# Kernel optimization log

Measured on AMD Instinct MI355X. Metric: run time of the kernel, lower is better.

Reference implementation:

```python
import jax, jax.numpy as jnp
import numpy as np

N = 20000          # num nodes
E = 250000         # num edges
B = 128            # num graphs in batch
Fin = 512
Fqk = 512
Fv = 512
H = 8              # nheads


def setup_inputs() -> dict:
    key = jax.random.key(0)
    k1, k2, k3, k4 = jax.random.split(key, 4)
    x = jax.random.normal(k1, (N, Fin), dtype=jnp.float32)
    batch = jnp.sort(jax.random.randint(k2, (N,), 0, B)).astype(jnp.int32)
    ei = jax.random.randint(k3, (2, E), 0, N).astype(jnp.int32)
    # proj weight of Linear(Fin, 2*Fqk+Fv, bias=False); stored as (Fin, Ftot)
    W = (jax.random.normal(k4, (Fin, 2 * Fqk + Fv), dtype=jnp.float32)
         / np.sqrt(Fin).astype(np.float32))
    return {"x": x, "batch": batch, "ei": ei, "W": W}


def reference(x, batch, ei, W):
    src, dest = ei[0], ei[1]
    n = x.shape[0]
    Fh = Fqk // H            # head dim for q/k
    Fhv = Fv // H            # head dim for v
    scaling = float(Fh) ** (-0.5)

    qkv = x @ W                                    # (N, 2*Fqk+Fv)
    q, k, v = jnp.split(qkv, [Fqk, 2 * Fqk], axis=-1)
    q = (q * scaling).reshape(n, H, Fh)
    k = k.reshape(n, H, Fh)
    v = v.reshape(n, H, Fhv)

    # edge-wise gathers
    qs = q[src]                                    # (E, H, Fh)
    ks = k[dest]                                   # (E, H, Fh)
    vs = v[dest]                                   # (E, H, Fhv)

    # per-edge, per-head attention scores
    aw = jnp.einsum('ehf,ehf->eh', qs, ks)         # (E, H)

    # segment softmax over edges sharing the same src node (stable)
    m = jax.ops.segment_max(aw, src, num_segments=n)       # (N, H)
    e = jnp.exp(aw - m[src])                                # (E, H)
    denom = jax.ops.segment_sum(e, src, num_segments=n)     # (N, H)
    alpha = e / denom[src]                                   # (E, H)

    # scatter-weighted aggregation of values back to src nodes
    out = jax.ops.segment_sum(alpha[:, :, None] * vs, src, num_segments=n)  # (N, H, Fhv)
    return out.reshape(n, Fv)
```

## Files before the change

### kernel.cpp

```cpp
#include <hip/hip_runtime.h>
#include <cstdint>

typedef float f32x4 __attribute__((ext_vector_type(4)));
typedef __bf16 bf16x8 __attribute__((ext_vector_type(8)));

__device__ __forceinline__ unsigned short f2b(float f) {
  unsigned int u = __float_as_uint(f);
  u = (u + 0x7fffu + ((u >> 16) & 1u)) >> 16;
  return (unsigned short)u;
}

__device__ __forceinline__ void unpack8(uint4 u, float* f) {
  f[0] = __uint_as_float((u.x & 0xffffu) << 16);
  f[1] = __uint_as_float(u.x & 0xffff0000u);
  f[2] = __uint_as_float((u.y & 0xffffu) << 16);
  f[3] = __uint_as_float(u.y & 0xffff0000u);
  f[4] = __uint_as_float((u.z & 0xffffu) << 16);
  f[5] = __uint_as_float(u.z & 0xffff0000u);
  f[6] = __uint_as_float((u.w & 0xffffu) << 16);
  f[7] = __uint_as_float(u.w & 0xffff0000u);
}

__device__ __forceinline__ void async_copy16(const void* g, void* l) {
  __builtin_amdgcn_global_load_lds(
      (const __attribute__((address_space(1))) void*)g,
      (__attribute__((address_space(3))) void*)l, 16, 0, 0);
}

__global__ __launch_bounds__(256) void prep_kernel(
    const float* __restrict__ W, unsigned short* __restrict__ Wt, int NT,
    const int* __restrict__ src, const int* __restrict__ dst,
    int* __restrict__ deg, int* __restrict__ edst, int E, int nbConvw) {
  __shared__ float tile[32][33];
  int bx = blockIdx.x, t = threadIdx.x;

  if (bx < nbConvw) {
    int b = bx;
    int tilesPerRow = NT / 32;
    int n0 = (b % tilesPerRow) * 32, k0 = (b / tilesPerRow) * 32;
    int r = t >> 5, c = t & 31;
#pragma unroll
    for (int ph = 0; ph < 4; ++ph)
      tile[r + 8 * ph][c] = W[(size_t)(k0 + r + 8 * ph) * NT + n0 + c];
    __syncthreads();
#pragma unroll
    for (int ph = 0; ph < 4; ++ph) {
      int rr = r + 8 * ph;
      int nn = n0 + rr;
      float s = (nn < 512) ? 0.125f : 1.0f;
      Wt[(size_t)nn * 512 + k0 + c] = f2b(tile[c][rr] * s);
    }
  } else {
    int e = (bx - nbConvw) * 256 + t;
    if (e < E) {
      int s = src[e], d = dst[e];
      int j = atomicAdd(&deg[s], 1);
      if (j < 64) edst[(size_t)s * 64 + j] = d;
    }
  }
}

__global__ __launch_bounds__(1024, 4) void gemm256_kernel(
    const float* __restrict__ X, const unsigned short* __restrict__ Bt,
    unsigned short* __restrict__ C, int K, int NT, int NPAN, int nrows) {
  __shared__ __align__(16) unsigned short SM[49152];

  int bx = blockIdx.x, tid = threadIdx.x;
  int nwg = gridDim.x;
  int q8 = nwg >> 3, r8 = nwg & 7;
  int xcd = bx & 7, idx = bx >> 3;
  int wgid = (xcd < r8 ? xcd * (q8 + 1) : r8 * (q8 + 1) + (xcd - r8) * q8) + idx;
  int mtile = wgid / NPAN, npanel = wgid % NPAN;
  int m0 = mtile * 256, n0 = npanel * 256;

  int wave = tid >> 6, lane = tid & 63;
  int wm = wave >> 2, wn = wave & 3;
  int hi = lane >> 4, l15 = lane & 15;

  int srow = (tid >> 6) * 16 + l15;
  int scol = ((tid >> 4) & 3) * 8;
  bool inb = (m0 + srow) < nrows;
  const float* pX = X + (size_t)(m0 + srow) * K + scol;
  const unsigned short* pB = Bt + (size_t)(n0 + srow) * K + scol;

  auto loadA = [&](int t, float4& f0, float4& f1) {
    if (inb) {
      f0 = *(const float4*)(pX + t * 32);
      f1 = *(const float4*)(pX + t * 32 + 4);
    } else {
      f0 = make_float4(0.f, 0.f, 0.f, 0.f);
      f1 = make_float4(0.f, 0.f, 0.f, 0.f);
    }
  };
  auto cvtWriteA = [&](const float4& f0, const float4& f1, int slot) {
    uint4 w;
    w.x = (unsigned)f2b(f0.x) | ((unsigned)f2b(f0.y) << 16);
    w.y = (unsigned)f2b(f0.z) | ((unsigned)f2b(f0.w) << 16);
    w.z = (unsigned)f2b(f1.x) | ((unsigned)f2b(f1.y) << 16);
    w.w = (unsigned)f2b(f1.z) | ((unsigned)f2b(f1.w) << 16);
    *(uint4*)(SM + slot * 8192 + tid * 8) = w;
  };

  async_copy16(pB, SM + 24576 + tid * 8);
  async_copy16(pB + 32, SM + 24576 + 8192 + tid * 8);
  __builtin_amdgcn_sched_barrier(0);
  float4 f00, f01, nf0, nf1;
  loadA(0, f00, f01);
  loadA(1, nf0, nf1);
  __builtin_amdgcn_sched_barrier(0);
  cvtWriteA(f00, f01, 0);
  asm volatile("s_waitcnt lgkmcnt(0)" ::: "memory");
  __builtin_amdgcn_s_barrier();
  __builtin_amdgcn_sched_barrier(0);

  f32x4 acc[4][4] = {};
  int aoff = wm * 2048 + lane * 8;
  int boff = 24576 + wn * 2048 + lane * 8;

#pragma unroll
  for (int t = 0; t < 16; ++t) {
    int sb = (t % 3) * 8192;
    bf16x8 av[4], bv[4];
    const unsigned short* a_ = SM + sb + aoff;
    const unsigned short* b_ = SM + sb + boff;
#pragma unroll
    for (int i = 0; i < 4; ++i) av[i] = *(const bf16x8*)(a_ + i * 512);
#pragma unroll
    for (int j = 0; j < 4; ++j) bv[j] = *(const bf16x8*)(b_ + j * 512);
    if (t + 2 < 16) {
      int s2 = ((t + 2) % 3) * 8192;
      async_copy16(pB + (t + 2) * 32, SM + 24576 + s2 + tid * 8);
    }
    if (t + 1 < 16) cvtWriteA(nf0, nf1, (t + 1) % 3);
    if (t + 2 < 16) loadA(t + 2, nf0, nf1);
    __builtin_amdgcn_s_setprio(1);
#pragma unroll
    for (int i = 0; i < 4; ++i)
#pragma unroll
      for (int j = 0; j < 4; ++j)
        acc[i][j] = __builtin_amdgcn_mfma_f32_16x16x32_bf16(av[i], bv[j], acc[i][j], 0, 0, 0);
    __builtin_amdgcn_s_setprio(0);
    if (t + 2 < 16) {
      asm volatile("s_waitcnt vmcnt(2)" ::: "memory");
    } else {
      asm volatile("s_waitcnt vmcnt(0)" ::: "memory");
    }
    asm volatile("s_waitcnt lgkmcnt(0)" ::: "memory");
    __builtin_amdgcn_sched_barrier(0);
    __builtin_amdgcn_s_barrier();
    __builtin_amdgcn_sched_barrier(0);
  }

  __syncthreads();
  unsigned short* cs = SM + wave * 640;
  unsigned short* gC = C + (size_t)(m0 + wm * 64) * NT + n0 + wn * 64;
  int erow = lane >> 2, echunk = (lane & 3) * 8;
#pragma unroll
  for (int i = 0; i < 4; ++i)
#pragma unroll
    for (int p = 0; p < 2; ++p) {
#pragma unroll
      for (int jj = 0; jj < 2; ++jj)
#pragma unroll
        for (int q = 0; q < 4; ++q)
          cs[(hi * 4 + q) * 40 + jj * 16 + l15] = f2b(acc[i][2 * p + jj][q]);
      uint4 val = *(const uint4*)&cs[erow * 40 + echunk];
      *(uint4*)&gC[(size_t)(i * 16 + erow) * NT + p * 32 + echunk] = val;
    }
}

__global__ __launch_bounds__(256) void attn_kernel(
    const unsigned short* __restrict__ qkv, const int* __restrict__ deg,
    const int* __restrict__ edst, float* __restrict__ out, int n) {
  int wave = threadIdx.x >> 6, lane = threadIdx.x & 63;
  int node = blockIdx.x * 4 + wave;
  if (node >= n) return;

  float q[8];
  unpack8(*(const uint4*)(qkv + (size_t)node * 1536 + lane * 8), q);

  float acc[8] = {0.f, 0.f, 0.f, 0.f, 0.f, 0.f, 0.f, 0.f};
  float l = 0.f;
  int dn = deg[node];
  if (dn > 64) dn = 64;
  int beg = node * 64, end = beg + dn;

  int i = beg;
  for (; i + 4 <= end; i += 4) {
    int d0 = edst[i], d1 = edst[i + 1], d2 = edst[i + 2], d3 = edst[i + 3];
    const uint4* p0 = (const uint4*)(qkv + (size_t)d0 * 1536 + 512 + lane * 8);
    const uint4* p1 = (const uint4*)(qkv + (size_t)d1 * 1536 + 512 + lane * 8);
    const uint4* p2 = (const uint4*)(qkv + (size_t)d2 * 1536 + 512 + lane * 8);
    const uint4* p3 = (const uint4*)(qkv + (size_t)d3 * 1536 + 512 + lane * 8);
    uint4 kr0 = p0[0], vr0 = p0[64];
    uint4 kr1 = p1[0], vr1 = p1[64];
    uint4 kr2 = p2[0], vr2 = p2[64];
    uint4 kr3 = p3[0], vr3 = p3[64];
#pragma unroll
    for (int u = 0; u < 4; ++u) {
      uint4 kv = (u == 0) ? kr0 : (u == 1) ? kr1 : (u == 2) ? kr2 : kr3;
      uint4 vv = (u == 0) ? vr0 : (u == 1) ? vr1 : (u == 2) ? vr2 : vr3;
      float kf[8], vf[8];
      unpack8(kv, kf);
      unpack8(vv, vf);
      float part = 0.f;
#pragma unroll
      for (int j = 0; j < 8; ++j) part = fmaf(q[j], kf[j], part);
      part += __shfl_xor(part, 1);
      part += __shfl_xor(part, 2);
      part += __shfl_xor(part, 4);
      float p = __expf(part);
      l += p;
#pragma unroll
      for (int j = 0; j < 8; ++j) acc[j] = fmaf(p, vf[j], acc[j]);
    }
  }
  for (; i < end; ++i) {
    int d = edst[i];
    const uint4* pp = (const uint4*)(qkv + (size_t)d * 1536 + 512 + lane * 8);
    uint4 kv = pp[0], vv = pp[64];
    float kf[8], vf[8];
    unpack8(kv, kf);
    unpack8(vv, vf);
    float part = 0.f;
#pragma unroll
    for (int j = 0; j < 8; ++j) part = fmaf(q[j], kf[j], part);
    part += __shfl_xor(part, 1);
    part += __shfl_xor(part, 2);
    part += __shfl_xor(part, 4);
    float p = __expf(part);
    l += p;
#pragma unroll
    for (int j = 0; j < 8; ++j) acc[j] = fmaf(p, vf[j], acc[j]);
  }

  float inv = (l > 0.f) ? 1.f / l : 0.f;
  float4 o0, o1;
  o0.x = acc[0] * inv; o0.y = acc[1] * inv; o0.z = acc[2] * inv; o0.w = acc[3] * inv;
  o1.x = acc[4] * inv; o1.y = acc[5] * inv; o1.z = acc[6] * inv; o1.w = acc[7] * inv;
  float4* op = (float4*)(out + (size_t)node * 512 + lane * 8);
  op[0] = o0;
  op[1] = o1;
}

extern "C" void kernel_launch(void* const* d_in, const int* in_sizes, int n_in,
                              void* d_out, int out_size, void* d_ws, size_t ws_size,
                              hipStream_t stream) {
  const float* x = (const float*)d_in[0];
  const int* ei = (const int*)d_in[2];
  const float* W = (const float*)d_in[3];
  float* out = (float*)d_out;

  const int N = in_sizes[1];
  const int E = in_sizes[2] / 2;
  const int Fin = in_sizes[0] / N;
  const int FT = in_sizes[3] / Fin;
  const int MPAD = ((N + 255) / 256) * 256;

  const int* src = ei;
  const int* dst = ei + E;

  char* ws = (char*)d_ws;
  size_t off = 0;
  auto alloc = [&](size_t bytes) {
    void* p = ws + off;
    off = (off + bytes + 255) & ~(size_t)255;
    return p;
  };
  unsigned short* Wt  = (unsigned short*)alloc((size_t)FT * Fin * 2);
  unsigned short* qkv = (unsigned short*)alloc((size_t)MPAD * FT * 2);
  int* deg  = (int*)alloc((size_t)N * 4);
  int* edst = (int*)alloc((size_t)N * 64 * 4);

  hipMemsetAsync(deg, 0, (size_t)N * 4, stream);

  int nbConvw = (FT / 32) * (Fin / 32);
  int nbBucket = (E + 255) / 256;
  prep_kernel<<<nbConvw + nbBucket, 256, 0, stream>>>(
      W, Wt, FT, src, dst, deg, edst, E, nbConvw);

  int NPAN = FT / 256;
  int MTILES = MPAD / 256;
  gemm256_kernel<<<MTILES * NPAN, 1024, 0, stream>>>(x, Wt, qkv, Fin, FT, NPAN, N);

  attn_kernel<<<(N + 3) / 4, 256, 0, stream>>>(qkv, deg, edst, out, N);
}
```

Measured before the change: 155.7 us.

## Move edge bucketing into GEMM launch and make attention grid-stride persistent

The edge-bucketing work (atomic degree count and adjacency fill) moves out of the weight-conversion kernel and into extra blocks appended to the GEMM launch. It then runs alongside the GEMM tiles instead of in front of them, which shortens the prep kernel. The attention kernel becomes a grid-stride loop over nodes with a fixed 1024 blocks instead of one wave per node. The bucketing blocks use 1024 threads under the GEMM's launch bounds and LDS allocation, which may limit how many can be resident.

```diff
diff --git a/kernel.cpp b/kernel.cpp
--- a/kernel.cpp
+++ b/kernel.cpp
@@ -28,45 +28,45 @@
 }
 
 __global__ __launch_bounds__(256) void prep_kernel(
-    const float* __restrict__ W, unsigned short* __restrict__ Wt, int NT,
-    const int* __restrict__ src, const int* __restrict__ dst,
-    int* __restrict__ deg, int* __restrict__ edst, int E, int nbConvw) {
+    const float* __restrict__ W, unsigned short* __restrict__ Wt, int NT) {
   __shared__ float tile[32][33];
-  int bx = blockIdx.x, t = threadIdx.x;
-
-  if (bx < nbConvw) {
-    int b = bx;
-    int tilesPerRow = NT / 32;
-    int n0 = (b % tilesPerRow) * 32, k0 = (b / tilesPerRow) * 32;
-    int r = t >> 5, c = t & 31;
-#pragma unroll
-    for (int ph = 0; ph < 4; ++ph)
-      tile[r + 8 * ph][c] = W[(size_t)(k0 + r + 8 * ph) * NT + n0 + c];
-    __syncthreads();
-#pragma unroll
-    for (int ph = 0; ph < 4; ++ph) {
-      int rr = r + 8 * ph;
-      int nn = n0 + rr;
-      float s = (nn < 512) ? 0.125f : 1.0f;
-      Wt[(size_t)nn * 512 + k0 + c] = f2b(tile[c][rr] * s);
-    }
-  } else {
-    int e = (bx - nbConvw) * 256 + t;
+  int b = blockIdx.x, t = threadIdx.x;
+  int tilesPerRow = NT / 32;
+  int n0 = (b % tilesPerRow) * 32, k0 = (b / tilesPerRow) * 32;
+  int r = t >> 5, c = t & 31;
+#pragma unroll
+  for (int ph = 0; ph < 4; ++ph)
+    tile[r + 8 * ph][c] = W[(size_t)(k0 + r + 8 * ph) * NT + n0 + c];
+  __syncthreads();
+#pragma unroll
+  for (int ph = 0; ph < 4; ++ph) {
+    int rr = r + 8 * ph;
+    int nn = n0 + rr;
+    float s = (nn < 512) ? 0.125f : 1.0f;
+    Wt[(size_t)nn * 512 + k0 + c] = f2b(tile[c][rr] * s);
+  }
+}
+
+__global__ __launch_bounds__(1024, 4) void gemm256_kernel(
+    const float* __restrict__ X, const unsigned short* __restrict__ Bt,
+    unsigned short* __restrict__ C, int K, int NT, int NPAN, int nrows,
+    int GEMMB, const int* __restrict__ src, const int* __restrict__ dst,
+    int* __restrict__ deg, int* __restrict__ edst, int E) {
+  __shared__ __align__(16) unsigned short SM[49152];
+
+  int bx = blockIdx.x, tid = threadIdx.x;
+
+  if (bx >= GEMMB) {
+    int e = (bx - GEMMB) * 1024 + tid;
     if (e < E) {
       int s = src[e], d = dst[e];
       int j = atomicAdd(&deg[s], 1);
       if (j < 64) edst[(size_t)s * 64 + j] = d;
     }
-  }
-}
-
-__global__ __launch_bounds__(1024, 4) void gemm256_kernel(
-    const float* __restrict__ X, const unsigned short* __restrict__ Bt,
-    unsigned short* __restrict__ C, int K, int NT, int NPAN, int nrows) {
-  __shared__ __align__(16) unsigned short SM[49152];
-
-  int bx = blockIdx.x, tid = threadIdx.x;
-  int nwg = gridDim.x;
+    return;
+  }
+
+  int nwg = GEMMB;
   int q8 = nwg >> 3, r8 = nwg & 7;
   int xcd = bx & 7, idx = bx >> 3;
   int wgid = (xcd < r8 ? xcd * (q8 + 1) : r8 * (q8 + 1) + (xcd - r8) * q8) + idx;
@@ -171,35 +171,54 @@
 
 __global__ __launch_bounds__(256) void attn_kernel(
     const unsigned short* __restrict__ qkv, const int* __restrict__ deg,
-    const int* __restrict__ edst, float* __restrict__ out, int n) {
-  int wave = threadIdx.x >> 6, lane = threadIdx.x & 63;
-  int node = blockIdx.x * 4 + wave;
-  if (node >= n) return;
-
-  float q[8];
-  unpack8(*(const uint4*)(qkv + (size_t)node * 1536 + lane * 8), q);
-
-  float acc[8] = {0.f, 0.f, 0.f, 0.f, 0.f, 0.f, 0.f, 0.f};
-  float l = 0.f;
-  int dn = deg[node];
-  if (dn > 64) dn = 64;
-  int beg = node * 64, end = beg + dn;
-
-  int i = beg;
-  for (; i + 4 <= end; i += 4) {
-    int d0 = edst[i], d1 = edst[i + 1], d2 = edst[i + 2], d3 = edst[i + 3];
-    const uint4* p0 = (const uint4*)(qkv + (size_t)d0 * 1536 + 512 + lane * 8);
-    const uint4* p1 = (const uint4*)(qkv + (size_t)d1 * 1536 + 512 + lane * 8);
-    const uint4* p2 = (const uint4*)(qkv + (size_t)d2 * 1536 + 512 + lane * 8);
-    const uint4* p3 = (const uint4*)(qkv + (size_t)d3 * 1536 + 512 + lane * 8);
-    uint4 kr0 = p0[0], vr0 = p0[64];
-    uint4 kr1 = p1[0], vr1 = p1[64];
-    uint4 kr2 = p2[0], vr2 = p2[64];
-    uint4 kr3 = p3[0], vr3 = p3[64];
-#pragma unroll
-    for (int u = 0; u < 4; ++u) {
-      uint4 kv = (u == 0) ? kr0 : (u == 1) ? kr1 : (u == 2) ? kr2 : kr3;
-      uint4 vv = (u == 0) ? vr0 : (u == 1) ? vr1 : (u == 2) ? vr2 : vr3;
+    const int* __restrict__ edst, float* __restrict__ out, int n, int nwtot) {
+  int gw = blockIdx.x * 4 + (threadIdx.x >> 6);
+  int lane = threadIdx.x & 63;
+
+  for (int node = gw; node < n; node += nwtot) {
+    float q[8];
+    unpack8(*(const uint4*)(qkv + (size_t)node * 1536 + lane * 8), q);
+
+    float acc[8] = {0.f, 0.f, 0.f, 0.f, 0.f, 0.f, 0.f, 0.f};
+    float l = 0.f;
+    int dn = deg[node];
+    if (dn > 64) dn = 64;
+    int beg = node * 64, end = beg + dn;
+
+    int i = beg;
+    for (; i + 4 <= end; i += 4) {
+      int d0 = edst[i], d1 = edst[i + 1], d2 = edst[i + 2], d3 = edst[i + 3];
+      const uint4* p0 = (const uint4*)(qkv + (size_t)d0 * 1536 + 512 + lane * 8);
+      const uint4* p1 = (const uint4*)(qkv + (size_t)d1 * 1536 + 512 + lane * 8);
+      const uint4* p2 = (const uint4*)(qkv + (size_t)d2 * 1536 + 512 + lane * 8);
+      const uint4* p3 = (const uint4*)(qkv + (size_t)d3 * 1536 + 512 + lane * 8);
+      uint4 kr0 = p0[0], vr0 = p0[64];
+      uint4 kr1 = p1[0], vr1 = p1[64];
+      uint4 kr2 = p2[0], vr2 = p2[64];
+      uint4 kr3 = p3[0], vr3 = p3[64];
+#pragma unroll
+      for (int u = 0; u < 4; ++u) {
+        uint4 kv = (u == 0) ? kr0 : (u == 1) ? kr1 : (u == 2) ? kr2 : kr3;
+        uint4 vv = (u == 0) ? vr0 : (u == 1) ? vr1 : (u == 2) ? vr2 : vr3;
+        float kf[8], vf[8];
+        unpack8(kv, kf);
+        unpack8(vv, vf);
+        float part = 0.f;
+#pragma unroll
+        for (int j = 0; j < 8; ++j) part = fmaf(q[j], kf[j], part);
+        part += __shfl_xor(part, 1);
+        part += __shfl_xor(part, 2);
+        part += __shfl_xor(part, 4);
+        float p = __expf(part);
+        l += p;
+#pragma unroll
+        for (int j = 0; j < 8; ++j) acc[j] = fmaf(p, vf[j], acc[j]);
+      }
+    }
+    for (; i < end; ++i) {
+      int d = edst[i];
+      const uint4* pp = (const uint4*)(qkv + (size_t)d * 1536 + 512 + lane * 8);
+      uint4 kv = pp[0], vv = pp[64];
       float kf[8], vf[8];
       unpack8(kv, kf);
       unpack8(vv, vf);
@@ -214,33 +233,15 @@
 #pragma unroll
       for (int j = 0; j < 8; ++j) acc[j] = fmaf(p, vf[j], acc[j]);
     }
-  }
-  for (; i < end; ++i) {
-    int d = edst[i];
-    const uint4* pp = (const uint4*)(qkv + (size_t)d * 1536 + 512 + lane * 8);
-    uint4 kv = pp[0], vv = pp[64];
-    float kf[8], vf[8];
-    unpack8(kv, kf);
-    unpack8(vv, vf);
-    float part = 0.f;
-#pragma unroll
-    for (int j = 0; j < 8; ++j) part = fmaf(q[j], kf[j], part);
-    part += __shfl_xor(part, 1);
-    part += __shfl_xor(part, 2);
-    part += __shfl_xor(part, 4);
-    float p = __expf(part);
-    l += p;
-#pragma unroll
-    for (int j = 0; j < 8; ++j) acc[j] = fmaf(p, vf[j], acc[j]);
-  }
-
-  float inv = (l > 0.f) ? 1.f / l : 0.f;
-  float4 o0, o1;
-  o0.x = acc[0] * inv; o0.y = acc[1] * inv; o0.z = acc[2] * inv; o0.w = acc[3] * inv;
-  o1.x = acc[4] * inv; o1.y = acc[5] * inv; o1.z = acc[6] * inv; o1.w = acc[7] * inv;
-  float4* op = (float4*)(out + (size_t)node * 512 + lane * 8);
-  op[0] = o0;
-  op[1] = o1;
+
+    float inv = (l > 0.f) ? 1.f / l : 0.f;
+    float4 o0, o1;
+    o0.x = acc[0] * inv; o0.y = acc[1] * inv; o0.z = acc[2] * inv; o0.w = acc[3] * inv;
+    o1.x = acc[4] * inv; o1.y = acc[5] * inv; o1.z = acc[6] * inv; o1.w = acc[7] * inv;
+    float4* op = (float4*)(out + (size_t)node * 512 + lane * 8);
+    op[0] = o0;
+    op[1] = o1;
+  }
 }
 
 extern "C" void kernel_launch(void* const* d_in, const int* in_sizes, int n_in,
@@ -275,13 +276,16 @@
   hipMemsetAsync(deg, 0, (size_t)N * 4, stream);
 
   int nbConvw = (FT / 32) * (Fin / 32);
-  int nbBucket = (E + 255) / 256;
-  prep_kernel<<<nbConvw + nbBucket, 256, 0, stream>>>(
-      W, Wt, FT, src, dst, deg, edst, E, nbConvw);
+  prep_kernel<<<nbConvw, 256, 0, stream>>>(W, Wt, FT);
 
   int NPAN = FT / 256;
   int MTILES = MPAD / 256;
-  gemm256_kernel<<<MTILES * NPAN, 1024, 0, stream>>>(x, Wt, qkv, Fin, FT, NPAN, N);
-
-  attn_kernel<<<(N + 3) / 4, 256, 0, stream>>>(qkv, deg, edst, out, N);
-}
+  int GEMMB = MTILES * NPAN;
+  int nbBucket = (E + 1023) / 1024;
+  gemm256_kernel<<<GEMMB + nbBucket, 1024, 0, stream>>>(
+      x, Wt, qkv, Fin, FT, NPAN, N, GEMMB, src, dst, deg, edst, E);
+
+  int attnBlocks = 1024;
+  attn_kernel<<<attnBlocks, 256, 0, stream>>>(qkv, deg, edst, out, N,
+                                              attnBlocks * 4);
+}
```

New measurement: 147.8 us. 5.1% less time.
